# Optimization experiments

Hardware: AMD Instinct MI355X
Metric: run time of the kernel (lower is better)

Reference implementation:

```python
import jax, jax.numpy as jnp
import numpy as np

N_NODES = 50000
NEG_SLOPE = 0.2


def gat_layer(x, src, dst, edge_attr, W, a_src, a_dst, We, a_edge, b, n):
    """PyG GATConv (heads=1, concat=True, add_self_loops=True, fill_value='mean')."""
    h = x @ W                                   # [N, C] shared lin for src/dst
    alpha_s = h @ a_src                          # [N]
    alpha_d = h @ a_dst                          # [N]
    # self loops; self-loop edge_attr = mean of incoming edge_attr per node
    deg = jax.ops.segment_sum(jnp.ones_like(dst, dtype=edge_attr.dtype), dst, num_segments=n)
    ea_mean = jax.ops.segment_sum(edge_attr, dst, num_segments=n) / jnp.maximum(deg, 1.0)[:, None]
    loop = jnp.arange(n, dtype=src.dtype)
    s = jnp.concatenate([src, loop])             # [E+N]
    d = jnp.concatenate([dst, loop])
    ea = jnp.concatenate([edge_attr, ea_mean], axis=0)
    alpha_e = (ea @ We) @ a_edge                 # [E+N]
    alpha = jax.nn.leaky_relu(alpha_s[s] + alpha_d[d] + alpha_e, NEG_SLOPE)
    # segment softmax over destination neighborhoods (self-loops guarantee non-empty)
    amax = jax.ops.segment_max(alpha, d, num_segments=n)
    ealpha = jnp.exp(alpha - amax[d])
    denom = jax.ops.segment_sum(ealpha, d, num_segments=n)
    coef = ealpha / denom[d]                     # [E+N]
    out = jax.ops.segment_sum(h[s] * coef[:, None], d, num_segments=n)
    return out + b


def setup_inputs() -> dict:
    key = jax.random.key(0)
    ks = jax.random.split(key, 16)
    N, E, F_in, H, C, ED = N_NODES, 800000, 256, 128, 128, 60
    inp = {
        "x": jax.random.normal(ks[0], (N, F_in), jnp.float32),
        "edge_index": jax.random.randint(ks[1], (2, E), 0, N, jnp.int32),
        "edge_features": jax.random.normal(ks[2], (E, ED), jnp.float32),
        "batch_size": 16,
    }
    def glorot(k, shape):
        fan = shape[0] + (shape[1] if len(shape) > 1 else 1)
        return jax.random.normal(k, shape, jnp.float32) * np.sqrt(2.0 / fan)
    # layer 1
    inp["W1"] = glorot(ks[3], (F_in, H))
    inp["a_src1"] = glorot(ks[4], (H,))
    inp["a_dst1"] = glorot(ks[5], (H,))
    inp["We1"] = glorot(ks[6], (ED, H))
    inp["a_edge1"] = glorot(ks[7], (H,))
    inp["b1"] = jnp.zeros((H,), jnp.float32)
    # layer 2
    inp["W2"] = glorot(ks[8], (H, C))
    inp["a_src2"] = glorot(ks[9], (C,))
    inp["a_dst2"] = glorot(ks[10], (C,))
    inp["We2"] = glorot(ks[11], (ED, C))
    inp["a_edge2"] = glorot(ks[12], (C,))
    inp["b2"] = jnp.zeros((C,), jnp.float32)
    return inp


def reference(x, edge_index, edge_features, batch_size,
              W1, a_src1, a_dst1, We1, a_edge1, b1,
              W2, a_src2, a_dst2, We2, a_edge2, b2):
    n = x.shape[0]
    src, dst = edge_index[0], edge_index[1]
    h = gat_layer(x, src, dst, edge_features, W1, a_src1, a_dst1, We1, a_edge1, b1, n)
    h = jax.nn.relu(h)
    z = gat_layer(h, src, dst, edge_features, W2, a_src2, a_dst2, We2, a_edge2, b2, n)
    # decode: gather-dot over labeled edge pairs
    res = jnp.sum(z[src] * z[dst], axis=-1)      # [E]
    half = res.shape[0] // 2
    res_half = res[:half] + res[half:]
    return res_half.reshape((batch_size, -1))
```

## Files before the change

kernel.cpp:

```cpp
#include <hip/hip_runtime.h>
#include <hip/hip_bf16.h>

typedef __attribute__((ext_vector_type(8))) short short8;
typedef __attribute__((ext_vector_type(4))) float floatx4;

__device__ __forceinline__ float wsum(float v){
  #pragma unroll
  for (int m = 32; m >= 1; m >>= 1) v += __shfl_xor(v, m);
  return v;
}
__device__ __forceinline__ float lrelu(float a){ return a > 0.f ? a : 0.2f * a; }
__device__ __forceinline__ float bflo(unsigned u){ return __uint_as_float(u << 16); }
__device__ __forceinline__ float bfhi(unsigned u){ return __uint_as_float(u & 0xffff0000u); }
__device__ __forceinline__ unsigned short f2bf(float f){
  __hip_bfloat16 h = __float2bfloat16(f);
  return *reinterpret_cast<unsigned short*>(&h);
}
__device__ __forceinline__ float dot4(float4 a, float4 b){
  return a.x*b.x + a.y*b.y + a.z*b.z + a.w*b.w;
}

__global__ __launch_bounds__(256) void k_prep(const int* __restrict__ dst, int* __restrict__ degi,
                       int* __restrict__ eslot, int E, int CB,
                       const float* __restrict__ We1, const float* __restrict__ ae1,
                       const float* __restrict__ We2, const float* __restrict__ ae2,
                       float* __restrict__ we1, float* __restrict__ we2,
                       const float* __restrict__ W1, unsigned short* __restrict__ W1t,
                       const float* __restrict__ W2, unsigned short* __restrict__ W2t) {
  int t = threadIdx.x;
  if (blockIdx.x < (unsigned)CB) {
    int e = blockIdx.x * 256 + t;
    if (e < E) eslot[e] = atomicAdd(degi + dst[e], 1);
    return;
  }
  int b = blockIdx.x - CB;
  if (b == 0) {
    if (t >= 64) return;
    float s1 = 0.f, s2 = 0.f;
    if (t < 60) {
      const float4* r1 = reinterpret_cast<const float4*>(We1 + t * 128);
      const float4* r2 = reinterpret_cast<const float4*>(We2 + t * 128);
      const float4* a1 = reinterpret_cast<const float4*>(ae1);
      const float4* a2 = reinterpret_cast<const float4*>(ae2);
      for (int i = 0; i < 32; ++i) {
        float4 x1 = r1[i], y1 = a1[i];
        float4 x2 = r2[i], y2 = a2[i];
        s1 += x1.x*y1.x + x1.y*y1.y + x1.z*y1.z + x1.w*y1.w;
        s2 += x2.x*y2.x + x2.y*y2.y + x2.z*y2.z + x2.w*y2.w;
      }
    }
    we1[t] = s1; we2[t] = s2;
  } else if (b <= 128) {
    int idx = (b - 1) * 256 + t;
    int k = idx >> 7, n = idx & 127;
    W1t[(size_t)n * 256 + k] = f2bf(W1[idx]);
  } else {
    int idx = (b - 129) * 256 + t;
    int k = idx >> 7, n = idx & 127;
    W2t[(size_t)n * 128 + k] = f2bf(W2[idx]);
  }
}

__global__ __launch_bounds__(1024) void k_scan(const int* __restrict__ degi, int* __restrict__ rowptr,
                                               int N, int E) {
  __shared__ int wsums[16];
  int t = threadIdx.x;
  int wave = t >> 6, lane = t & 63;
  const int CH = 52;
  int lo = t * CH;
  int v[52];
  int s = 0;
  #pragma unroll
  for (int i = 0; i < 13; ++i) {
    int base_i = lo + 4 * i;
    if (base_i + 4 <= N) {
      int4 q = *reinterpret_cast<const int4*>(degi + base_i);
      v[4*i+0] = q.x; v[4*i+1] = q.y; v[4*i+2] = q.z; v[4*i+3] = q.w;
      s += q.x + q.y + q.z + q.w;
    } else {
      #pragma unroll
      for (int j = 0; j < 4; ++j) {
        int idx = base_i + j;
        int x = (idx < N) ? degi[idx] : 0;
        v[4*i+j] = x; s += x;
      }
    }
  }
  int inc = s;
  #pragma unroll
  for (int off = 1; off < 64; off <<= 1) {
    int u = __shfl_up(inc, off);
    if (lane >= off) inc += u;
  }
  if (lane == 63) wsums[wave] = inc;
  __syncthreads();
  if (wave == 0) {
    int ws = (lane < 16) ? wsums[lane] : 0;
    #pragma unroll
    for (int off = 1; off < 16; off <<= 1) {
      int u = __shfl_up(ws, off);
      if (lane >= off) ws += u;
    }
    if (lane < 16) wsums[lane] = ws;
  }
  __syncthreads();
  int base = inc - s + (wave ? wsums[wave - 1] : 0);
  #pragma unroll
  for (int i = 0; i < 13; ++i) {
    int base_i = lo + 4 * i;
    if (base_i + 4 <= N) {
      int4 o;
      o.x = base; base += v[4*i+0];
      o.y = base; base += v[4*i+1];
      o.z = base; base += v[4*i+2];
      o.w = base; base += v[4*i+3];
      *reinterpret_cast<int4*>(rowptr + base_i) = o;
    } else {
      #pragma unroll
      for (int j = 0; j < 4; ++j) {
        int idx = base_i + j;
        if (idx < N) { rowptr[idx] = base; base += v[4*i+j]; }
      }
    }
  }
  if (t == 0) rowptr[N] = E;
}

template <int K, bool AFP32>
__device__ __forceinline__ void gemm_body(int wid, int lane,
    const void* __restrict__ Av, const unsigned short* __restrict__ Bt,
    unsigned short* __restrict__ C,
    const float* __restrict__ a_src, const float* __restrict__ a_dst,
    float* __restrict__ alps, float* __restrict__ alpd, int M) {
  int mt = wid;
  if (mt * 16 >= M) return;
  int r = lane & 15, quad = lane >> 4;
  int m = mt * 16 + r;
  floatx4 acc[8] = {};
  for (int k0 = 0; k0 < K; k0 += 32) {
    int kk = k0 + quad * 8;
    short8 a;
    if (AFP32) {
      const float4* ap = reinterpret_cast<const float4*>((const float*)Av + (size_t)m * K + kk);
      float4 lo = ap[0], hi = ap[1];
      union { short8 v; unsigned short u[8]; } pa;
      pa.u[0]=f2bf(lo.x); pa.u[1]=f2bf(lo.y); pa.u[2]=f2bf(lo.z); pa.u[3]=f2bf(lo.w);
      pa.u[4]=f2bf(hi.x); pa.u[5]=f2bf(hi.y); pa.u[6]=f2bf(hi.z); pa.u[7]=f2bf(hi.w);
      a = pa.v;
    } else {
      a = *reinterpret_cast<const short8*>((const unsigned short*)Av + (size_t)m * K + kk);
    }
    #pragma unroll
    for (int t = 0; t < 8; ++t) {
      short8 b = *reinterpret_cast<const short8*>(Bt + (size_t)(t*16 + r) * K + kk);
      acc[t] = __builtin_amdgcn_mfma_f32_16x16x32_bf16(a, b, acc[t], 0, 0, 0);
    }
  }
  float asv[8], adv[8];
  #pragma unroll
  for (int t = 0; t < 8; ++t) {
    int col = t * 16 + r;
    asv[t] = a_src[col]; adv[t] = a_dst[col];
  }
  #pragma unroll
  for (int rr = 0; rr < 4; ++rr) {
    float ps = 0.f, pd = 0.f;
    #pragma unroll
    for (int t = 0; t < 8; ++t) { ps += acc[t][rr] * asv[t]; pd += acc[t][rr] * adv[t]; }
    #pragma unroll
    for (int mo = 1; mo <= 8; mo <<= 1) { ps += __shfl_xor(ps, mo); pd += __shfl_xor(pd, mo); }
    if (r == 0) {
      int row = mt * 16 + quad * 4 + rr;
      alps[row] = ps;
      alpd[row] = pd;
    }
  }
  #pragma unroll
  for (int t = 0; t < 8; ++t) {
    int col = t * 16 + r;
    #pragma unroll
    for (int rr = 0; rr < 4; ++rr) {
      int row = mt * 16 + quad * 4 + rr;
      C[(size_t)row * 128 + col] = f2bf(acc[t][rr]);
    }
  }
}

template <int K, bool AFP32>
__global__ __launch_bounds__(256) void k_gemm(const void* __restrict__ Av, const unsigned short* __restrict__ Bt,
                                              unsigned short* __restrict__ C,
                                              const float* __restrict__ a_src, const float* __restrict__ a_dst,
                                              float* __restrict__ alps, float* __restrict__ alpd, int M) {
  int wid = (blockIdx.x * 256 + threadIdx.x) >> 6;
  int lane = threadIdx.x & 63;
  gemm_body<K, AFP32>(wid, lane, Av, Bt, C, a_src, a_dst, alps, alpd, M);
}

__device__ __forceinline__ void fill_body(int fb, int t, int FILLB,
    const int* __restrict__ src, const int* __restrict__ dst,
    const float* __restrict__ ef,
    const float* __restrict__ we1, const float* __restrict__ we2,
    const int* __restrict__ rowptr, const int* __restrict__ eslot,
    float4* __restrict__ csr, int E) {
  int sub = t & 3;
  int qw = fb * 64 + (t >> 2);
  int QWT = FILLB * 64;
  int CH = (E + QWT - 1) / QWT;
  int eBeg = qw * CH;
  if (eBeg >= E) return;
  int eEnd = eBeg + CH; if (eEnd > E) eEnd = E;

  const float4* w1v = reinterpret_cast<const float4*>(we1);
  const float4* w2v = reinterpret_cast<const float4*>(we2);
  float4 wa0 = w1v[sub],     wb0 = w2v[sub];
  float4 wa1 = w1v[sub + 4], wb1 = w2v[sub + 4];
  float4 wa2 = w1v[sub + 8], wb2 = w2v[sub + 8];
  float4 wa3, wb3;
  if (sub == 3) { wa3 = make_float4(0.f,0.f,0.f,0.f); wb3 = wa3; }
  else          { wa3 = w1v[sub + 12]; wb3 = w2v[sub + 12]; }
  int i3off = (sub == 3) ? 0 : sub + 12;

  const float4* efq = reinterpret_cast<const float4*>(ef);
  int e = eBeg;
  size_t b = (size_t)e * 15;
  float4 f0 = efq[b + sub], f1 = efq[b + sub + 4], f2 = efq[b + sub + 8];
  float4 f3 = efq[b + i3off];
  int svc = src[e], dc = dst[e], sc = eslot[e];
  int rpc = rowptr[dc];
  while (e < eEnd) {
    int en = e + 1;
    bool hasN = en < eEnd;
    float4 g0, g1, g2, g3;
    int svn = 0, dn = 0, sn = 0;
    if (hasN) {
      size_t bn = (size_t)en * 15;
      g0 = efq[bn + sub]; g1 = efq[bn + sub + 4]; g2 = efq[bn + sub + 8];
      g3 = efq[bn + i3off];
      svn = src[en]; dn = dst[en]; sn = eslot[en];
    }
    float d1 = dot4(f0, wa0) + dot4(f1, wa1) + dot4(f2, wa2) + dot4(f3, wa3);
    float d2 = dot4(f0, wb0) + dot4(f1, wb1) + dot4(f2, wb2) + dot4(f3, wb3);
    d1 += __shfl_xor(d1, 1); d1 += __shfl_xor(d1, 2);
    d2 += __shfl_xor(d2, 1); d2 += __shfl_xor(d2, 2);
    int rpn = hasN ? rowptr[dn] : 0;
    if (sub == 0) {
      float4 v;
      v.x = __int_as_float(svc); v.y = d1; v.z = d2; v.w = 0.f;
      csr[rpc + sc] = v;
    }
    e = en;
    f0 = g0; f1 = g1; f2 = g2; f3 = g3;
    svc = svn; dc = dn; sc = sn; rpc = rpn;
  }
}

__global__ __launch_bounds__(256) void k_fillgemm(
                       const int* __restrict__ src, const int* __restrict__ dst,
                       const float* __restrict__ ef,
                       const float* __restrict__ we1, const float* __restrict__ we2,
                       const int* __restrict__ rowptr, const int* __restrict__ eslot,
                       float4* __restrict__ csr, int E, int GB, int FILLB,
                       const float* __restrict__ x, const unsigned short* __restrict__ W1t,
                       unsigned short* __restrict__ hA,
                       const float* __restrict__ a_src, const float* __restrict__ a_dst,
                       float* __restrict__ alps, float* __restrict__ alpd, int N) {
  int t = threadIdx.x;
  if (blockIdx.x < (unsigned)GB) {
    int wid = (blockIdx.x * 256 + t) >> 6;
    int lane = t & 63;
    gemm_body<256, true>(wid, lane, x, W1t, hA, a_src, a_dst, alps, alpd, N);
    return;
  }
  fill_body(blockIdx.x - GB, t, FILLB, src, dst, ef, we1, we2, rowptr, eslot, csr, E);
}

__global__ __launch_bounds__(256) void k_agg(const int* __restrict__ rowptr, const float4* __restrict__ csr,
                      const float* __restrict__ as_, const float* __restrict__ ad_,
                      const unsigned short* __restrict__ h, const float* __restrict__ bias,
                      unsigned short* __restrict__ out, int N, int use2, int do_relu) {
  int i = (blockIdx.x * blockDim.x + threadIdx.x) >> 6;
  int lane = threadIdx.x & 63;
  if (i >= N) return;
  int st = lane >> 4;
  int q  = lane & 15;
  int start = rowptr[i], end = rowptr[i + 1];
  int cnt = end - start;
  float adi = ad_[i], asi = as_[i];
  float m = -3.0e38f, s = 0.f, esum = 0.f;
  float acc[8] = {};
  int idx = start + st;
  float4 cur, nx;
  float as_c = 0.f; uint4 hv_c;
  if (idx < end) {
    cur = csr[idx];
    int sv = __float_as_int(cur.x);
    as_c = as_[sv];
    hv_c = *reinterpret_cast<const uint4*>(h + (size_t)sv * 128 + q * 8);
  }
  if (idx + 4 < end) nx = csr[idx + 4];
  for (; idx < end; idx += 4) {
    float4 n2;
    if (idx + 8 < end) n2 = csr[idx + 8];
    float as_n = 0.f; uint4 hv_n;
    if (idx + 4 < end) {
      int svn = __float_as_int(nx.x);
      as_n = as_[svn];
      hv_n = *reinterpret_cast<const uint4*>(h + (size_t)svn * 128 + q * 8);
    }
    float e = use2 ? cur.z : cur.y;
    float a = lrelu(as_c + adi + e);
    esum += e;
    if (a > m + 8.f) {
      float rr = __expf(m - a);
      s *= rr;
      #pragma unroll
      for (int j = 0; j < 8; ++j) acc[j] *= rr;
      m = a;
    }
    float w = __expf(a - m);
    s += w;
    acc[0] += w * bflo(hv_c.x); acc[1] += w * bfhi(hv_c.x);
    acc[2] += w * bflo(hv_c.y); acc[3] += w * bfhi(hv_c.y);
    acc[4] += w * bflo(hv_c.z); acc[5] += w * bfhi(hv_c.z);
    acc[6] += w * bflo(hv_c.w); acc[7] += w * bfhi(hv_c.w);
    cur = nx; nx = n2; as_c = as_n; hv_c = hv_n;
  }
  #pragma unroll
  for (int off = 16; off <= 32; off <<= 1) {
    float m_o = __shfl_xor(m, off);
    float s_o = __shfl_xor(s, off);
    float e_o = __shfl_xor(esum, off);
    float ao[8];
    #pragma unroll
    for (int j = 0; j < 8; ++j) ao[j] = __shfl_xor(acc[j], off);
    float Mn = fmaxf(m, m_o);
    float f  = __expf(m - Mn), fo = __expf(m_o - Mn);
    s = s * f + s_o * fo;
    #pragma unroll
    for (int j = 0; j < 8; ++j) acc[j] = acc[j] * f + ao[j] * fo;
    esum += e_o;
    m = Mn;
  }
  float a_self = lrelu(asi + adi + esum / fmaxf((float)cnt, 1.f));
  float M2 = fmaxf(m, a_self);
  float g = __expf(m - M2);
  float w_self = __expf(a_self - M2);
  s = s * g + w_self;
  uint4 hs = *reinterpret_cast<const uint4*>(h + (size_t)i * 128 + q * 8);
  float hsf[8] = { bflo(hs.x), bfhi(hs.x), bflo(hs.y), bfhi(hs.y),
                   bflo(hs.z), bfhi(hs.z), bflo(hs.w), bfhi(hs.w) };
  #pragma unroll
  for (int j = 0; j < 8; ++j) acc[j] = acc[j] * g + w_self * hsf[j];
  float inv = 1.0f / s;
  float4 bv0 = *reinterpret_cast<const float4*>(bias + q * 8);
  float4 bv1 = *reinterpret_cast<const float4*>(bias + q * 8 + 4);
  float o[8];
  o[0] = acc[0]*inv + bv0.x; o[1] = acc[1]*inv + bv0.y;
  o[2] = acc[2]*inv + bv0.z; o[3] = acc[3]*inv + bv0.w;
  o[4] = acc[4]*inv + bv1.x; o[5] = acc[5]*inv + bv1.y;
  o[6] = acc[6]*inv + bv1.z; o[7] = acc[7]*inv + bv1.w;
  if (do_relu) {
    #pragma unroll
    for (int j = 0; j < 8; ++j) o[j] = fmaxf(o[j], 0.f);
  }
  if (st == 0) {
    uint4 ov;
    ov.x = (unsigned)f2bf(o[0]) | ((unsigned)f2bf(o[1]) << 16);
    ov.y = (unsigned)f2bf(o[2]) | ((unsigned)f2bf(o[3]) << 16);
    ov.z = (unsigned)f2bf(o[4]) | ((unsigned)f2bf(o[5]) << 16);
    ov.w = (unsigned)f2bf(o[6]) | ((unsigned)f2bf(o[7]) << 16);
    *reinterpret_cast<uint4*>(out + (size_t)i * 128 + q * 8) = ov;
  }
}

__global__ void k_decode(const int* __restrict__ src, const int* __restrict__ dst,
                         const unsigned short* __restrict__ z, float* __restrict__ out, int halfE) {
  int w = (blockIdx.x * blockDim.x + threadIdx.x) >> 6;
  int lane = threadIdx.x & 63;
  int k0 = w * 4;
  if (k0 >= halfE) return;
  int g = lane >> 3;
  int q = lane & 7;
  int r = g >> 1, hh = g & 1;
  int k = k0 + r;
  float p = 0.f;
  if (k < halfE) {
    int e = k + hh * halfE;
    int sv = src[e], dv = dst[e];
    const uint4* za = reinterpret_cast<const uint4*>(z + (size_t)sv * 128 + q * 16);
    const uint4* zb = reinterpret_cast<const uint4*>(z + (size_t)dv * 128 + q * 16);
    uint4 a0 = za[0], a1 = za[1];
    uint4 b0 = zb[0], b1 = zb[1];
    p = bflo(a0.x)*bflo(b0.x) + bfhi(a0.x)*bfhi(b0.x)
      + bflo(a0.y)*bflo(b0.y) + bfhi(a0.y)*bfhi(b0.y)
      + bflo(a0.z)*bflo(b0.z) + bfhi(a0.z)*bfhi(b0.z)
      + bflo(a0.w)*bflo(b0.w) + bfhi(a0.w)*bfhi(b0.w)
      + bflo(a1.x)*bflo(b1.x) + bfhi(a1.x)*bfhi(b1.x)
      + bflo(a1.y)*bflo(b1.y) + bfhi(a1.y)*bfhi(b1.y)
      + bflo(a1.z)*bflo(b1.z) + bfhi(a1.z)*bfhi(b1.z)
      + bflo(a1.w)*bflo(b1.w) + bfhi(a1.w)*bfhi(b1.w);
  }
  p += __shfl_xor(p, 1);
  p += __shfl_xor(p, 2);
  p += __shfl_xor(p, 4);
  p += __shfl_xor(p, 8);
  if ((lane & 15) == 0) {
    int kk = k0 + (lane >> 4);
    if (kk < halfE) out[kk] = p;
  }
}

extern "C" void kernel_launch(void* const* d_in, const int* in_sizes, int n_in,
                              void* d_out, int out_size, void* d_ws, size_t ws_size,
                              hipStream_t stream) {
  const int H = 128;
  const int N = in_sizes[0] / 256;
  const int E = in_sizes[1] / 2;
  const int half = E / 2;

  const float* x   = (const float*)d_in[0];
  const int* eidx  = (const int*)d_in[1];
  const float* ef  = (const float*)d_in[2];
  const float* W1  = (const float*)d_in[4];
  const float* as1 = (const float*)d_in[5];
  const float* ad1 = (const float*)d_in[6];
  const float* We1 = (const float*)d_in[7];
  const float* ae1 = (const float*)d_in[8];
  const float* b1  = (const float*)d_in[9];
  const float* W2  = (const float*)d_in[10];
  const float* as2 = (const float*)d_in[11];
  const float* ad2 = (const float*)d_in[12];
  const float* We2 = (const float*)d_in[13];
  const float* ae2 = (const float*)d_in[14];
  const float* b2  = (const float*)d_in[15];

  const int* src = eidx;
  const int* dst = eidx + E;

  size_t off = 0;
  auto alloc = [&](size_t bytes) -> void* {
    void* p = (char*)d_ws + off;
    off += (bytes + 255) & ~(size_t)255;
    return p;
  };
  float*  we1    = (float*)alloc(64 * 4);
  float*  we2    = (float*)alloc(64 * 4);
  int*    degi   = (int*)alloc((size_t)N * 4);
  float*  alps   = (float*)alloc((size_t)N * 4);
  float*  alpd   = (float*)alloc((size_t)N * 4);
  int*    eslot  = (int*)alloc((size_t)E * 4);
  int*    rowptr = (int*)alloc((size_t)(N + 1) * 4);
  float4* csr    = (float4*)alloc((size_t)E * 16);
  unsigned short* W1t = (unsigned short*)alloc((size_t)128 * 256 * 2);
  unsigned short* W2t = (unsigned short*)alloc((size_t)128 * 128 * 2);
  unsigned short* hA  = (unsigned short*)alloc((size_t)N * H * 2);
  unsigned short* hB  = (unsigned short*)alloc((size_t)N * H * 2);

  hipMemsetAsync(degi, 0, (size_t)N * 4, stream);

  int CB = (E + 255) / 256;
  k_prep<<<CB + 193, 256, 0, stream>>>(dst, degi, eslot, E, CB,
                                       We1, ae1, We2, ae2, we1, we2, W1, W1t, W2, W2t);
  k_scan<<<1, 1024, 0, stream>>>(degi, rowptr, N, E);

  int gwaves = (N + 15) / 16;
  int GB = (gwaves + 3) / 4;
  int FILLB = 2500;
  k_fillgemm<<<GB + FILLB, 256, 0, stream>>>(src, dst, ef, we1, we2, rowptr, eslot, csr,
                                             E, GB, FILLB,
                                             x, W1t, hA, as1, ad1, alps, alpd, N);
  k_agg<<<(N + 3) / 4, 256, 0, stream>>>(rowptr, csr, alps, alpd, hA, b1, hB, N, 0, 1);
  k_gemm<128, false><<<GB, 256, 0, stream>>>(hB, W2t, hA, as2, ad2, alps, alpd, N);
  k_agg<<<(N + 3) / 4, 256, 0, stream>>>(rowptr, csr, alps, alpd, hA, b2, hB, N, 1, 0);
  int dwaves = (half + 3) / 4;
  k_decode<<<(dwaves + 3) / 4, 256, 0, stream>>>(src, dst, hB, (float*)d_out, half);
}
```

Measured before the change: 571.8 us.

## Move edge-feature dot products into scan kernel, simplify CSR scatter

The per-edge attention dot products over the 60-wide edge features now run in extra blocks launched alongside the single-block prefix scan, which previously left most of the GPU idle. Results go to a new float2 buffer. The CSR fill then becomes a simple one-thread-per-edge scatter fused with the first GEMM. This removes the serial per-thread edge loop from the fill kernel and overlaps the edge-feature streaming with the scan. The cost is an extra E*8-byte buffer written and read back.

```diff
diff --git a/kernel.cpp b/kernel.cpp
--- a/kernel.cpp
+++ b/kernel.cpp
@@ -4,11 +4,6 @@
 typedef __attribute__((ext_vector_type(8))) short short8;
 typedef __attribute__((ext_vector_type(4))) float floatx4;
 
-__device__ __forceinline__ float wsum(float v){
-  #pragma unroll
-  for (int m = 32; m >= 1; m >>= 1) v += __shfl_xor(v, m);
-  return v;
-}
 __device__ __forceinline__ float lrelu(float a){ return a > 0.f ? a : 0.2f * a; }
 __device__ __forceinline__ float bflo(unsigned u){ return __uint_as_float(u << 16); }
 __device__ __forceinline__ float bfhi(unsigned u){ return __uint_as_float(u & 0xffff0000u); }
@@ -61,8 +56,8 @@
   }
 }
 
-__global__ __launch_bounds__(1024) void k_scan(const int* __restrict__ degi, int* __restrict__ rowptr,
-                                               int N, int E) {
+__device__ __forceinline__ void scan_body(const int* __restrict__ degi, int* __restrict__ rowptr,
+                                          int N, int E) {
   __shared__ int wsums[16];
   int t = threadIdx.x;
   int wave = t >> 6, lane = t & 63;
@@ -124,6 +119,40 @@
     }
   }
   if (t == 0) rowptr[N] = E;
+}
+
+__global__ __launch_bounds__(1024) void k_scanedot(const int* __restrict__ degi, int* __restrict__ rowptr,
+                       int N, int E,
+                       const float* __restrict__ ef,
+                       const float* __restrict__ we1, const float* __restrict__ we2,
+                       float2* __restrict__ edgeD, int EDOTB) {
+  if (blockIdx.x == 0) { scan_body(degi, rowptr, N, E); return; }
+  int t = threadIdx.x;
+  int sub = t & 3;
+  int qw = (int)(blockIdx.x - 1) * 256 + (t >> 2);
+  const float4* w1v = reinterpret_cast<const float4*>(we1);
+  const float4* w2v = reinterpret_cast<const float4*>(we2);
+  float4 wa0 = w1v[sub],     wb0 = w2v[sub];
+  float4 wa1 = w1v[sub + 4], wb1 = w2v[sub + 4];
+  float4 wa2 = w1v[sub + 8], wb2 = w2v[sub + 8];
+  bool has3 = sub < 3;
+  float4 wa3 = make_float4(0.f,0.f,0.f,0.f), wb3 = wa3;
+  if (has3) { wa3 = w1v[sub + 12]; wb3 = w2v[sub + 12]; }
+  const float4* efq = reinterpret_cast<const float4*>(ef);
+  int stride = EDOTB * 256;
+  for (int e = qw; e < E; e += stride) {
+    size_t b = (size_t)e * 15;
+    float4 f0 = efq[b + sub];
+    float4 f1 = efq[b + sub + 4];
+    float4 f2 = efq[b + sub + 8];
+    float4 f3 = make_float4(0.f,0.f,0.f,0.f);
+    if (has3) f3 = efq[b + sub + 12];
+    float d1 = dot4(f0, wa0) + dot4(f1, wa1) + dot4(f2, wa2) + dot4(f3, wa3);
+    float d2 = dot4(f0, wb0) + dot4(f1, wb1) + dot4(f2, wb2) + dot4(f3, wb3);
+    d1 += __shfl_xor(d1, 1); d1 += __shfl_xor(d1, 2);
+    d2 += __shfl_xor(d2, 1); d2 += __shfl_xor(d2, 2);
+    if (sub == 0) edgeD[e] = make_float2(d1, d2);
+  }
 }
 
 template <int K, bool AFP32>
@@ -196,70 +225,11 @@
   gemm_body<K, AFP32>(wid, lane, Av, Bt, C, a_src, a_dst, alps, alpd, M);
 }
 
-__device__ __forceinline__ void fill_body(int fb, int t, int FILLB,
-    const int* __restrict__ src, const int* __restrict__ dst,
-    const float* __restrict__ ef,
-    const float* __restrict__ we1, const float* __restrict__ we2,
-    const int* __restrict__ rowptr, const int* __restrict__ eslot,
-    float4* __restrict__ csr, int E) {
-  int sub = t & 3;
-  int qw = fb * 64 + (t >> 2);
-  int QWT = FILLB * 64;
-  int CH = (E + QWT - 1) / QWT;
-  int eBeg = qw * CH;
-  if (eBeg >= E) return;
-  int eEnd = eBeg + CH; if (eEnd > E) eEnd = E;
-
-  const float4* w1v = reinterpret_cast<const float4*>(we1);
-  const float4* w2v = reinterpret_cast<const float4*>(we2);
-  float4 wa0 = w1v[sub],     wb0 = w2v[sub];
-  float4 wa1 = w1v[sub + 4], wb1 = w2v[sub + 4];
-  float4 wa2 = w1v[sub + 8], wb2 = w2v[sub + 8];
-  float4 wa3, wb3;
-  if (sub == 3) { wa3 = make_float4(0.f,0.f,0.f,0.f); wb3 = wa3; }
-  else          { wa3 = w1v[sub + 12]; wb3 = w2v[sub + 12]; }
-  int i3off = (sub == 3) ? 0 : sub + 12;
-
-  const float4* efq = reinterpret_cast<const float4*>(ef);
-  int e = eBeg;
-  size_t b = (size_t)e * 15;
-  float4 f0 = efq[b + sub], f1 = efq[b + sub + 4], f2 = efq[b + sub + 8];
-  float4 f3 = efq[b + i3off];
-  int svc = src[e], dc = dst[e], sc = eslot[e];
-  int rpc = rowptr[dc];
-  while (e < eEnd) {
-    int en = e + 1;
-    bool hasN = en < eEnd;
-    float4 g0, g1, g2, g3;
-    int svn = 0, dn = 0, sn = 0;
-    if (hasN) {
-      size_t bn = (size_t)en * 15;
-      g0 = efq[bn + sub]; g1 = efq[bn + sub + 4]; g2 = efq[bn + sub + 8];
-      g3 = efq[bn + i3off];
-      svn = src[en]; dn = dst[en]; sn = eslot[en];
-    }
-    float d1 = dot4(f0, wa0) + dot4(f1, wa1) + dot4(f2, wa2) + dot4(f3, wa3);
-    float d2 = dot4(f0, wb0) + dot4(f1, wb1) + dot4(f2, wb2) + dot4(f3, wb3);
-    d1 += __shfl_xor(d1, 1); d1 += __shfl_xor(d1, 2);
-    d2 += __shfl_xor(d2, 1); d2 += __shfl_xor(d2, 2);
-    int rpn = hasN ? rowptr[dn] : 0;
-    if (sub == 0) {
-      float4 v;
-      v.x = __int_as_float(svc); v.y = d1; v.z = d2; v.w = 0.f;
-      csr[rpc + sc] = v;
-    }
-    e = en;
-    f0 = g0; f1 = g1; f2 = g2; f3 = g3;
-    svc = svn; dc = dn; sc = sn; rpc = rpn;
-  }
-}
-
-__global__ __launch_bounds__(256) void k_fillgemm(
+__global__ __launch_bounds__(256) void k_scatgemm(
                        const int* __restrict__ src, const int* __restrict__ dst,
-                       const float* __restrict__ ef,
-                       const float* __restrict__ we1, const float* __restrict__ we2,
-                       const int* __restrict__ rowptr, const int* __restrict__ eslot,
-                       float4* __restrict__ csr, int E, int GB, int FILLB,
+                       const int* __restrict__ eslot, const int* __restrict__ rowptr,
+                       const float2* __restrict__ edgeD, float4* __restrict__ csr,
+                       int E, int GB,
                        const float* __restrict__ x, const unsigned short* __restrict__ W1t,
                        unsigned short* __restrict__ hA,
                        const float* __restrict__ a_src, const float* __restrict__ a_dst,
@@ -271,7 +241,14 @@
     gemm_body<256, true>(wid, lane, x, W1t, hA, a_src, a_dst, alps, alpd, N);
     return;
   }
-  fill_body(blockIdx.x - GB, t, FILLB, src, dst, ef, we1, we2, rowptr, eslot, csr, E);
+  int e = (blockIdx.x - GB) * 256 + t;
+  if (e >= E) return;
+  int d = dst[e];
+  float2 dd = edgeD[e];
+  int slot = rowptr[d] + eslot[e];
+  float4 v;
+  v.x = __int_as_float(src[e]); v.y = dd.x; v.z = dd.y; v.w = 0.f;
+  csr[slot] = v;
 }
 
 __global__ __launch_bounds__(256) void k_agg(const int* __restrict__ rowptr, const float4* __restrict__ csr,
@@ -450,6 +427,7 @@
   float*  alpd   = (float*)alloc((size_t)N * 4);
   int*    eslot  = (int*)alloc((size_t)E * 4);
   int*    rowptr = (int*)alloc((size_t)(N + 1) * 4);
+  float2* edgeD  = (float2*)alloc((size_t)E * 8);
   float4* csr    = (float4*)alloc((size_t)E * 16);
   unsigned short* W1t = (unsigned short*)alloc((size_t)128 * 256 * 2);
   unsigned short* W2t = (unsigned short*)alloc((size_t)128 * 128 * 2);
@@ -461,14 +439,15 @@
   int CB = (E + 255) / 256;
   k_prep<<<CB + 193, 256, 0, stream>>>(dst, degi, eslot, E, CB,
                                        We1, ae1, We2, ae2, we1, we2, W1, W1t, W2, W2t);
-  k_scan<<<1, 1024, 0, stream>>>(degi, rowptr, N, E);
+
+  int EDOTB = 782;
+  k_scanedot<<<1 + EDOTB, 1024, 0, stream>>>(degi, rowptr, N, E, ef, we1, we2, edgeD, EDOTB);
 
   int gwaves = (N + 15) / 16;
   int GB = (gwaves + 3) / 4;
-  int FILLB = 2500;
-  k_fillgemm<<<GB + FILLB, 256, 0, stream>>>(src, dst, ef, we1, we2, rowptr, eslot, csr,
-                                             E, GB, FILLB,
-                                             x, W1t, hA, as1, ad1, alps, alpd, N);
+  int SB = (E + 255) / 256;
+  k_scatgemm<<<GB + SB, 256, 0, stream>>>(src, dst, eslot, rowptr, edgeD, csr, E, GB,
+                                          x, W1t, hA, as1, ad1, alps, alpd, N);
   k_agg<<<(N + 3) / 4, 256, 0, stream>>>(rowptr, csr, alps, alpd, hA, b1, hB, N, 0, 1);
   k_gemm<128, false><<<GB, 256, 0, stream>>>(hB, W2t, hA, as2, ad2, alps, alpd, N);
   k_agg<<<(N + 3) / 4, 256, 0, stream>>>(rowptr, csr, alps, alpd, hA, b2, hB, N, 1, 0);
```

Result: no change. 562.4 us (-1.6%).
